# Performance work log

Measured on AMD Instinct MI355X. Metric: run time of the kernel, lower is better.

## Reference

```python
import jax, jax.numpy as jnp
import numpy as np

B, T, D, H, NL = 8, 1024, 512, 8, 3
WS = (3, 5, 7)


def _mha(q_in, k_in, v_in, wq, bq, wk, bk, wv, bv, wo, bo):
    """Faithful copy of the torch MultiHeadAttention, including the
    transpose-free .view(B*H, -1, dh) head split (row-major reshape)."""
    bs = q_in.shape[0]
    dh = D // H
    q = (q_in @ wq + bq).reshape(bs * H, -1, dh)
    k = (k_in @ wk + bk).reshape(bs * H, -1, dh)
    v = (v_in @ wv + bv).reshape(bs * H, -1, dh)
    scores = jnp.einsum('bqd,bkd->bqk', q, k) / (dh ** 0.5)
    weights = jax.nn.softmax(scores, axis=-1)
    att = jnp.einsum('bqk,bkd->bqd', weights, v).reshape(bs, -1, D)
    return att @ wo + bo


def _forward(x, loc_wq, loc_bq, loc_wk, loc_bk, loc_wv, loc_bv, loc_wo, loc_bo,
             g_wq, g_bq, g_wk, g_bk, g_wv, g_bv, g_wo, g_bo, out_w, out_b):
    feats = []
    for lv in range(NL):
        w = WS[lv]
        pad = (w - 1) // 2
        xp = jnp.pad(x, ((0, 0), (pad, pad), (0, 0)))  # [B, T+2p, D]
        idx = jnp.arange(T)[:, None] + jnp.arange(w)[None, :]  # [T, w]
        win = xp[:, idx, :].reshape(B * T, w, D)  # sliding windows, same as unfold+permute
        lo = _mha(win, win, win,
                  loc_wq[lv], loc_bq[lv], loc_wk[lv], loc_bk[lv],
                  loc_wv[lv], loc_bv[lv], loc_wo[lv], loc_bo[lv])
        feats.append(lo.reshape(B, T, w, D).mean(axis=2))
    feats.append(_mha(x, x, x, g_wq, g_bq, g_wk, g_bk, g_wv, g_bv, g_wo, g_bo))
    combined = jnp.concatenate(feats, axis=-1)  # [B, T, D*(NL+1)]
    return combined @ out_w + out_b  # dropout is identity in eval mode


def setup_inputs() -> dict:
    key = jax.random.key(0)
    ks = jax.random.split(key, 20)
    s = 0.02
    d = {}
    d['x'] = jax.random.normal(ks[0], (B, T, D), jnp.float32)
    d['loc_wq'] = jax.random.normal(ks[1], (NL, D, D), jnp.float32) * s
    d['loc_bq'] = jax.random.normal(ks[2], (NL, D), jnp.float32) * s
    d['loc_wk'] = jax.random.normal(ks[3], (NL, D, D), jnp.float32) * s
    d['loc_bk'] = jax.random.normal(ks[4], (NL, D), jnp.float32) * s
    d['loc_wv'] = jax.random.normal(ks[5], (NL, D, D), jnp.float32) * s
    d['loc_bv'] = jax.random.normal(ks[6], (NL, D), jnp.float32) * s
    d['loc_wo'] = jax.random.normal(ks[7], (NL, D, D), jnp.float32) * s
    d['loc_bo'] = jax.random.normal(ks[8], (NL, D), jnp.float32) * s
    d['g_wq'] = jax.random.normal(ks[9], (D, D), jnp.float32) * s
    d['g_bq'] = jax.random.normal(ks[10], (D,), jnp.float32) * s
    d['g_wk'] = jax.random.normal(ks[11], (D, D), jnp.float32) * s
    d['g_bk'] = jax.random.normal(ks[12], (D,), jnp.float32) * s
    d['g_wv'] = jax.random.normal(ks[13], (D, D), jnp.float32) * s
    d['g_bv'] = jax.random.normal(ks[14], (D,), jnp.float32) * s
    d['g_wo'] = jax.random.normal(ks[15], (D, D), jnp.float32) * s
    d['g_bo'] = jax.random.normal(ks[16], (D,), jnp.float32) * s
    d['out_w'] = jax.random.normal(ks[17], (D * (NL + 1), D), jnp.float32) * s
    d['out_b'] = jax.random.normal(ks[18], (D,), jnp.float32) * s
    return d


def reference(x, loc_wq, loc_bq, loc_wk, loc_bk, loc_wv, loc_bv, loc_wo, loc_bo,
              g_wq, g_bq, g_wk, g_bk, g_wv, g_bv, g_wo, g_bo, out_w, out_b):
    return _forward(x, loc_wq, loc_bq, loc_wk, loc_bk, loc_wv, loc_bv, loc_wo, loc_bo,
                    g_wq, g_bq, g_wk, g_bk, g_wv, g_bv, g_wo, g_bo, out_w, out_b)
```

## Files before the change

kernel.cpp:

```cpp
#include <hip/hip_runtime.h>
#include <hip/hip_bf16.h>
#include <cstddef>

#define T_SEQ 1024
#define D_MODEL 512

typedef __attribute__((ext_vector_type(8))) __bf16 bf16x8;
typedef __attribute__((ext_vector_type(4))) float f32x4;
typedef __attribute__((ext_vector_type(16))) float f32x16;
typedef __attribute__((ext_vector_type(8))) unsigned short u16x8;
typedef __attribute__((ext_vector_type(4))) unsigned int u32x4;

typedef const unsigned int __attribute__((address_space(1)))* gas1_t;
typedef unsigned int __attribute__((address_space(3)))* las3_t;

__device__ __forceinline__ void gload_lds16(const void* g, void* l) {
  __builtin_amdgcn_global_load_lds((gas1_t)g, (las3_t)l, 16, 0, 0);
}

__device__ __forceinline__ float bf2f(unsigned short u) {
  return __uint_as_float(((unsigned)u) << 16);
}
__device__ __forceinline__ unsigned short f2bf(float f) {
  __hip_bfloat16 h = __float2bfloat16(f);
  return *(unsigned short*)&h;
}

#define CVTPK(dst, a, b) \
  asm("v_cvt_pk_bf16_f32 %0, %1, %2" : "=v"(dst) : "v"(a), "v"(b))

__device__ __forceinline__ void swap32(unsigned& a, unsigned& b, int lane) {
  const unsigned ax = __shfl_xor(a, 32);
  const unsigned bx = __shfl_xor(b, 32);
  const bool lo = lane < 32;
  const unsigned na = lo ? a : bx;
  const unsigned nb = lo ? ax : b;
  a = na; b = nb;
}

__global__ __launch_bounds__(256)
void prep_weights_kernel(const float* __restrict__ loc_wq, const float* __restrict__ loc_wk,
                         const float* __restrict__ loc_wv, const float* __restrict__ g_wq,
                         const float* __restrict__ g_wk, const float* __restrict__ g_wv,
                         const float* __restrict__ out_w, const float* __restrict__ loc_wo,
                         const float* __restrict__ g_wo, const float* __restrict__ x,
                         const float* __restrict__ loc_bq, const float* __restrict__ loc_bk,
                         const float* __restrict__ loc_bv,
                         __hip_bfloat16* __restrict__ WT, __hip_bfloat16* __restrict__ xb,
                         __hip_bfloat16* __restrict__ bqkvb) {
  __shared__ float tile[32][33];
  const size_t MS = (size_t)512 * 512;
  const int z = blockIdx.y;
  const int t = threadIdx.x;

  if (z == 20) {
    const int base = blockIdx.x * 16384 + t * 8;
#pragma unroll
    for (int it = 0; it < 8; ++it) {
      const int i = base + it * 2048;
      const float4 a = *(const float4*)(x + i);
      const float4 b = *(const float4*)(x + i + 4);
      u16x8 o;
      o[0] = f2bf(a.x); o[1] = f2bf(a.y); o[2] = f2bf(a.z); o[3] = f2bf(a.w);
      o[4] = f2bf(b.x); o[5] = f2bf(b.y); o[6] = f2bf(b.z); o[7] = f2bf(b.w);
      *(u16x8*)(xb + i) = o;
    }
    return;
  }
  if (z == 21) {
    const int i = blockIdx.x * 256 + t;
    if (blockIdx.x < 18) {
      const int which = i >> 9, lv = which / 3, role = which % 3, e = i & 511;
      const float* src = role == 0 ? loc_bq : role == 1 ? loc_bk : loc_bv;
      bqkvb[i] = __float2bfloat16(src[lv * 512 + e]);
    }
    return;
  }

  const float* src;
  bool tr = true;
  if (z < 3)       src = loc_wq + (size_t)z * MS;
  else if (z < 6)  src = loc_wk + (size_t)(z - 3) * MS;
  else if (z < 9)  src = loc_wv + (size_t)(z - 6) * MS;
  else if (z == 9)  src = g_wq;
  else if (z == 10) src = g_wk;
  else if (z == 11) src = g_wv;
  else if (z < 16) src = out_w + (size_t)(z - 12) * MS;
  else if (z < 19) { src = loc_wo + (size_t)(z - 16) * MS; tr = false; }
  else             { src = g_wo; tr = false; }
  __hip_bfloat16* dst = WT + (size_t)z * MS;

  const int tk = (blockIdx.x & 15) * 32;
  const int tn = (blockIdx.x >> 4) * 32;
  const int r = t >> 3, c4 = (t & 7) * 4;
  const float4 v = *(const float4*)(src + (size_t)(tk + r) * 512 + tn + c4);
  if (tr) {
    tile[r][c4 + 0] = v.x; tile[r][c4 + 1] = v.y;
    tile[r][c4 + 2] = v.z; tile[r][c4 + 3] = v.w;
    __syncthreads();
    ushort4 o;
    o.x = f2bf(tile[c4 + 0][r]); o.y = f2bf(tile[c4 + 1][r]);
    o.z = f2bf(tile[c4 + 2][r]); o.w = f2bf(tile[c4 + 3][r]);
    *(ushort4*)(dst + (size_t)(tn + r) * 512 + tk + c4) = o;
  } else {
    ushort4 o;
    o.x = f2bf(v.x); o.y = f2bf(v.y); o.z = f2bf(v.z); o.w = f2bf(v.w);
    *(ushort4*)(dst + (size_t)(tk + r) * 512 + tn + c4) = o;
  }
}

__global__ __launch_bounds__(256)
void bias_fuse_kernel(const float* __restrict__ loc_bo, const float* __restrict__ g_bo,
                      const float* __restrict__ out_w, const float* __restrict__ out_b,
                      float* __restrict__ bfused) {
  const int z = blockIdx.y;
  const int n = blockIdx.x * 256 + threadIdx.x;
  const float* bo = (z < 3) ? loc_bo + z * 512 : g_bo;
  const float* W = out_w + (size_t)z * 512 * 512;
  float acc = (z == 0) ? out_b[n] : 0.f;
  for (int m = 0; m < 512; ++m)
    acc = fmaf(bo[m], W[(size_t)m * 512 + n], acc);
  bfused[z * 512 + n] = acc;
}

__device__ __forceinline__ void gemm_core_b128(
    const __hip_bfloat16* __restrict__ A, const __hip_bfloat16* __restrict__ BT,
    __hip_bfloat16* As, __hip_bfloat16* Bs, int row0, int col0, f32x4 acc[4][4]) {
  const int tid = threadIdx.x;
  const int wv = tid >> 6, lane = tid & 63;
  const int g = lane >> 4, r16 = lane & 15;
  const int wm = wv >> 1, wn = wv & 1;
  const char* Ab = (const char*)A;
  const char* Bb = (const char*)BT;
  for (int k0 = 0; k0 < 512; k0 += 32) {
    {
      const int row = tid >> 2, off = (tid & 3) << 4;
      gload_lds16(Ab + (size_t)(row0 + row) * 1024 + k0 * 2 + off,
                  (char*)As + (wv << 10));
      const int i2 = tid + 256;
      const int row2 = i2 >> 2, off2 = (i2 & 3) << 4;
      gload_lds16(Ab + (size_t)(row0 + row2) * 1024 + k0 * 2 + off2,
                  (char*)As + 4096 + (wv << 10));
    }
    {
      const int row = tid >> 2, off = (tid & 3) << 4;
      gload_lds16(Bb + (size_t)(col0 + row) * 1024 + k0 * 2 + off,
                  (char*)Bs + (wv << 10));
      const int i2 = tid + 256;
      const int row2 = i2 >> 2, off2 = (i2 & 3) << 4;
      gload_lds16(Bb + (size_t)(col0 + row2) * 1024 + k0 * 2 + off2,
                  (char*)Bs + 4096 + (wv << 10));
    }
    __syncthreads();
    bf16x8 a[4], b[4];
#pragma unroll
    for (int m = 0; m < 4; ++m)
      a[m] = *(const bf16x8*)(As + (wm * 64 + m * 16 + r16) * 32 + g * 8);
#pragma unroll
    for (int n = 0; n < 4; ++n)
      b[n] = *(const bf16x8*)(Bs + (wn * 64 + n * 16 + r16) * 32 + g * 8);
#pragma unroll
    for (int m = 0; m < 4; ++m)
#pragma unroll
      for (int n = 0; n < 4; ++n)
        acc[m][n] = __builtin_amdgcn_mfma_f32_16x16x32_bf16(a[m], b[n], acc[m][n], 0, 0, 0);
    __syncthreads();
  }
}

__device__ __forceinline__ void gemm_core_b64(
    const __hip_bfloat16* __restrict__ A, const __hip_bfloat16* __restrict__ BT,
    __hip_bfloat16* As, __hip_bfloat16* Bs, int row0, int col0, f32x4 acc[2][4]) {
  const int tid = threadIdx.x;
  const int wv = tid >> 6, lane = tid & 63;
  const int g = lane >> 4, r16 = lane & 15;
  const int wm = wv >> 1, wn = wv & 1;
  const char* Ab = (const char*)A;
  const char* Bb = (const char*)BT;
  for (int k0 = 0; k0 < 512; k0 += 32) {
    {
      const int row = tid >> 2, off = (tid & 3) << 4;
      gload_lds16(Ab + (size_t)(row0 + row) * 1024 + k0 * 2 + off,
                  (char*)As + (wv << 10));
    }
    {
      const int row = tid >> 2, off = (tid & 3) << 4;
      gload_lds16(Bb + (size_t)(col0 + row) * 1024 + k0 * 2 + off,
                  (char*)Bs + (wv << 10));
      const int i2 = tid + 256;
      const int row2 = i2 >> 2, off2 = (i2 & 3) << 4;
      gload_lds16(Bb + (size_t)(col0 + row2) * 1024 + k0 * 2 + off2,
                  (char*)Bs + 4096 + (wv << 10));
    }
    __syncthreads();
    bf16x8 a[2], b[4];
#pragma unroll
    for (int m = 0; m < 2; ++m)
      a[m] = *(const bf16x8*)(As + (wm * 32 + m * 16 + r16) * 32 + g * 8);
#pragma unroll
    for (int n = 0; n < 4; ++n)
      b[n] = *(const bf16x8*)(Bs + (wn * 64 + n * 16 + r16) * 32 + g * 8);
#pragma unroll
    for (int m = 0; m < 2; ++m)
#pragma unroll
      for (int n = 0; n < 4; ++n)
        acc[m][n] = __builtin_amdgcn_mfma_f32_16x16x32_bf16(a[m], b[n], acc[m][n], 0, 0, 0);
    __syncthreads();
  }
}

__global__ __launch_bounds__(256)
void gemm_qkv_kernel(const __hip_bfloat16* __restrict__ A,
                     const __hip_bfloat16* __restrict__ WT_base, size_t wt_stride,
                     const float* __restrict__ b0, const float* __restrict__ b1,
                     const float* __restrict__ b2,
                     __hip_bfloat16* __restrict__ out_base) {
  __shared__ __attribute__((aligned(16))) __hip_bfloat16 As[4096];
  __shared__ __attribute__((aligned(16))) __hip_bfloat16 Bs[4096];
  const int z = blockIdx.z;
  const __hip_bfloat16* WT = WT_base + (size_t)z * wt_stride;
  const float* bias = (z == 0) ? b0 : (z == 1) ? b1 : b2;
  __hip_bfloat16* C = out_base + (size_t)z * (size_t)(8192 * 512);
  const int row0 = blockIdx.y * 128, col0 = blockIdx.x * 128;
  f32x4 acc[4][4];
#pragma unroll
  for (int m = 0; m < 4; ++m)
#pragma unroll
    for (int n = 0; n < 4; ++n) acc[m][n] = (f32x4)(0.0f);
  gemm_core_b128(A, WT, As, Bs, row0, col0, acc);
  const int lane = threadIdx.x & 63, wv = threadIdx.x >> 6;
  const int g = lane >> 4, r16 = lane & 15, wm = wv >> 1, wn = wv & 1;
#pragma unroll
  for (int n = 0; n < 4; ++n) {
    const int col = col0 + wn * 64 + n * 16 + r16;
    const float bn = bias[col];
#pragma unroll
    for (int m = 0; m < 4; ++m) {
      const int rowb = row0 + wm * 64 + m * 16 + g * 4;
#pragma unroll
      for (int r = 0; r < 4; ++r)
        C[(size_t)(rowb + r) * 512 + col] = __float2bfloat16(acc[m][n][r] + bn);
    }
  }
}

__global__ __launch_bounds__(256)
void gemm_fusew_kernel(const __hip_bfloat16* __restrict__ A_base,
                       const __hip_bfloat16* __restrict__ BT_base,
                       __hip_bfloat16* __restrict__ C_base) {
  __shared__ __attribute__((aligned(16))) __hip_bfloat16 As[4096];
  __shared__ __attribute__((aligned(16))) __hip_bfloat16 Bs[4096];
  const size_t MS = (size_t)512 * 512;
  const int z = blockIdx.z;
  const __hip_bfloat16* A = A_base + z * MS;
  const __hip_bfloat16* BT = BT_base + z * MS;
  __hip_bfloat16* C = C_base + z * MS;
  const int row0 = blockIdx.y * 128, col0 = blockIdx.x * 128;
  f32x4 acc[4][4];
#pragma unroll
  for (int m = 0; m < 4; ++m)
#pragma unroll
    for (int n = 0; n < 4; ++n) acc[m][n] = (f32x4)(0.0f);
  gemm_core_b128(A, BT, As, Bs, row0, col0, acc);
  const int lane = threadIdx.x & 63, wv = threadIdx.x >> 6;
  const int g = lane >> 4, r16 = lane & 15, wm = wv >> 1, wn = wv & 1;
#pragma unroll
  for (int n = 0; n < 4; ++n) {
    const int col = col0 + wn * 64 + n * 16 + r16;
#pragma unroll
    for (int m = 0; m < 4; ++m) {
      const int rowb = row0 + wm * 64 + m * 16 + g * 4;
#pragma unroll
      for (int r = 0; r < 4; ++r)
        C[(size_t)(rowb + r) * 512 + col] = __float2bfloat16(acc[m][n][r]);
    }
  }
}

__global__ __launch_bounds__(256)
void gemm_out_fused_kernel(const __hip_bfloat16* __restrict__ A0,
                           const __hip_bfloat16* __restrict__ A1,
                           const __hip_bfloat16* __restrict__ A2,
                           const __hip_bfloat16* __restrict__ A3,
                           const __hip_bfloat16* __restrict__ WT_base,
                           const float* __restrict__ bfused,
                           float* __restrict__ out) {
  __shared__ __attribute__((aligned(16))) __hip_bfloat16 As[2048];
  __shared__ __attribute__((aligned(16))) __hip_bfloat16 Bs[4096];
  const size_t MS = (size_t)512 * 512;
  const int row0 = blockIdx.y * 64, col0 = blockIdx.x * 128;
  f32x4 acc[2][4];
#pragma unroll
  for (int m = 0; m < 2; ++m)
#pragma unroll
    for (int n = 0; n < 4; ++n) acc[m][n] = (f32x4)(0.0f);
  const __hip_bfloat16* Az[4] = {A0, A1, A2, A3};
  for (int z = 0; z < 4; ++z)
    gemm_core_b64(Az[z], WT_base + (size_t)z * MS, As, Bs, row0, col0, acc);
  const int lane = threadIdx.x & 63, wv = threadIdx.x >> 6;
  const int g = lane >> 4, r16 = lane & 15, wm = wv >> 1, wn = wv & 1;
#pragma unroll
  for (int n = 0; n < 4; ++n) {
    const int col = col0 + wn * 64 + n * 16 + r16;
    const float bn = bfused[col] + bfused[512 + col] + bfused[1024 + col] +
                     bfused[1536 + col];
#pragma unroll
    for (int m = 0; m < 2; ++m) {
      const int rowb = row0 + wm * 32 + m * 16 + g * 4;
#pragma unroll
      for (int r = 0; r < 4; ++r)
        out[(size_t)(rowb + r) * 512 + col] = acc[m][n][r] + bn;
    }
  }
}

template <int W>
__device__ __forceinline__ const __hip_bfloat16* slot_row(
    const __hip_bfloat16* __restrict__ X, const __hip_bfloat16* __restrict__ biasb,
    int b, int tloc, int pg, int sl, int* ch_out) {
  constexpr int PAD = (W - 1) / 2;
  const int hloc = sl >> 3, p = sl & 7;
  const int m = (pg * 4 + hloc) * W + p;
  const int j = m >> 3;
  *ch_out = m & 7;
  int sr = tloc + j - PAD;
  if (p < W) {
    if (sr >= 0 && sr < T_SEQ) return X + ((size_t)(b * T_SEQ + sr) << 9);
    return biasb;
  }
  sr = sr < 0 ? 0 : (sr > T_SEQ - 1 ? T_SEQ - 1 : sr);
  return X + ((size_t)(b * T_SEQ + sr) << 9);
}

template <int W>
__global__ __launch_bounds__(256)
void local_attn_mfma_kernel(const __hip_bfloat16* __restrict__ Xq,
                            const __hip_bfloat16* __restrict__ Xk,
                            const __hip_bfloat16* __restrict__ Xv,
                            const __hip_bfloat16* __restrict__ bqb,
                            const __hip_bfloat16* __restrict__ bkb,
                            const __hip_bfloat16* __restrict__ bvb,
                            __hip_bfloat16* __restrict__ abar) {
  __shared__ unsigned lds_u[4][2048];
  const int tid = threadIdx.x;
  const int wv = tid >> 6, lane = tid & 63;
  const int bt = blockIdx.x * 4 + wv;
  const int b = bt >> 10, tloc = bt & 1023;
  unsigned* L = &lds_u[wv][0];
  const int dl = lane & 31, hi = lane >> 5;

  {
    const int k2 = dl, dhalf = hi;
    int ch0, ch1;
    const __hip_bfloat16* r0 =
        slot_row<W>(Xv, bvb, b, tloc, (2 * k2) >> 5, (2 * k2) & 31, &ch0);
    const __hip_bfloat16* r1 =
        slot_row<W>(Xv, bvb, b, tloc, (2 * k2 + 1) >> 5, (2 * k2 + 1) & 31, &ch1);
    u16x8 A0[4], A1[4];
#pragma unroll
    for (int q = 0; q < 4; ++q) {
      A0[q] = *(const u16x8*)(r0 + ch0 * 64 + dhalf * 32 + q * 8);
      A1[q] = *(const u16x8*)(r1 + ch1 * 64 + dhalf * 32 + q * 8);
    }
#pragma unroll
    for (int q = 0; q < 4; ++q)
#pragma unroll
      for (int e = 0; e < 8; ++e) {
        const int d_ = dhalf * 32 + q * 8 + e;
        const unsigned dw = (unsigned)A0[q][e] | ((unsigned)A1[q][e] << 16);
        const int byte = (d_ * 128 + k2 * 4) ^ ((d_ & 7) << 4);
        L[byte >> 2] = dw;
      }
  }

  f32x16 accP[2][2];
#pragma unroll
  for (int pg = 0; pg < 2; ++pg)
#pragma unroll
    for (int dh = 0; dh < 2; ++dh) accP[pg][dh] = (f32x16)(0.0f);

  const int myb = dl >> 3;

#pragma unroll
  for (int pg = 0; pg < 2; ++pg) {
    int chK, chQ;
    const __hip_bfloat16* rK = slot_row<W>(Xk, bkb, b, tloc, pg, dl, &chK);
    const __hip_bfloat16* rQ = slot_row<W>(Xq, bqb, b, tloc, pg, dl, &chQ);
    f32x16 sa = (f32x16)(0.0f);
#pragma unroll
    for (int i = 0; i < 4; ++i) {
      const bf16x8 kf = *(const bf16x8*)(rK + chK * 64 + i * 16 + hi * 8);
      const bf16x8 qf = *(const bf16x8*)(rQ + chQ * 64 + i * 16 + hi * 8);
      sa = __builtin_amdgcn_mfma_f32_32x32x16_bf16(kf, qf, sa, 0, 0, 0);
    }

    float sel[4];
#pragma unroll
    for (int r4 = 0; r4 < 4; ++r4)
      sel[r4] = (myb == 0) ? sa[r4]
              : (myb == 1) ? sa[4 + r4]
              : (myb == 2) ? sa[8 + r4] : sa[12 + r4];

    float mx = -3e38f;
#pragma unroll
    for (int r4 = 0; r4 < 4; ++r4)
      if (r4 + 4 * hi < W) mx = fmaxf(mx, sel[r4]);
    mx = fmaxf(mx, __shfl_xor(mx, 32));
    float e[4], ls = 0.f;
#pragma unroll
    for (int r4 = 0; r4 < 4; ++r4) {
      e[r4] = (r4 + 4 * hi < W) ? __expf(0.125f * (sel[r4] - mx)) : 0.f;
      ls += e[r4];
    }
    ls += __shfl_xor(ls, 32);
    const float inv = 1.f / ls;

    unsigned dw0, dw1;
    CVTPK(dw0, e[0] * inv, e[1] * inv);
    CVTPK(dw1, e[2] * inv, e[3] * inv);
    const unsigned q0 = __shfl_xor(dw0, 32);
    const unsigned q1 = __shfl_xor(dw1, 32);

#pragma unroll
    for (int kh = 0; kh < 2; ++kh) {
      const bool on = (2 * kh + hi) == myb;
      u32x4 bw;
      if (hi == 0) { bw[0] = dw0; bw[1] = dw1; bw[2] = q0; bw[3] = q1; }
      else         { bw[0] = q0;  bw[1] = q1;  bw[2] = dw0; bw[3] = dw1; }
      if (!on) { bw[0] = 0u; bw[1] = 0u; bw[2] = 0u; bw[3] = 0u; }
      const bf16x8 pf = __builtin_bit_cast(bf16x8, bw);
#pragma unroll
      for (int dh = 0; dh < 2; ++dh) {
        const int d_ = dh * 32 + dl;
        const int off = (d_ * 128 + pg * 64 + kh * 32 + hi * 16) ^ ((d_ & 7) << 4);
        const bf16x8 va =
            __builtin_bit_cast(bf16x8, *(const u32x4*)((const char*)L + off));
        accP[pg][dh] = __builtin_amdgcn_mfma_f32_32x32x16_bf16(va, pf, accP[pg][dh], 0, 0, 0);
      }
    }
  }

#pragma unroll
  for (int pg = 0; pg < 2; ++pg) {
    if ((dl & 7) < W) {
      const int m_o = (pg * 4 + (dl >> 3)) * W + (dl & 7);
#pragma unroll
      for (int dh = 0; dh < 2; ++dh) {
#pragma unroll
        for (int rq = 0; rq < 4; ++rq) {
          unsigned wa, wb;
          CVTPK(wa, accP[pg][dh][4 * rq + 0], accP[pg][dh][4 * rq + 1]);
          CVTPK(wb, accP[pg][dh][4 * rq + 2], accP[pg][dh][4 * rq + 3]);
          const int dwi = m_o * 34 + dh * 16 + rq * 4 + hi * 2;
          uint2 w; w.x = wa; w.y = wb;
          *(uint2*)(L + dwi) = w;
        }
      }
    }
  }
  asm volatile("s_waitcnt lgkmcnt(0)" ::: "memory");

  const int cho = lane >> 3, fb = lane & 7;
  float o[8] = {0.f, 0.f, 0.f, 0.f, 0.f, 0.f, 0.f, 0.f};
#pragma unroll
  for (int jj = 0; jj < W; ++jj) {
    const int mo = 8 * jj + cho;
    const uint2 w0 = *(const uint2*)(L + mo * 34 + fb * 4);
    const uint2 w1 = *(const uint2*)(L + mo * 34 + fb * 4 + 2);
    o[0] += bf2f((unsigned short)(w0.x & 0xffff));
    o[1] += bf2f((unsigned short)(w0.x >> 16));
    o[2] += bf2f((unsigned short)(w0.y & 0xffff));
    o[3] += bf2f((unsigned short)(w0.y >> 16));
    o[4] += bf2f((unsigned short)(w1.x & 0xffff));
    o[5] += bf2f((unsigned short)(w1.x >> 16));
    o[6] += bf2f((unsigned short)(w1.y & 0xffff));
    o[7] += bf2f((unsigned short)(w1.y >> 16));
  }
  const float invw = 1.f / (float)W;
  u16x8 ov;
#pragma unroll
  for (int e2 = 0; e2 < 8; ++e2) ov[e2] = f2bf(o[e2] * invw);
  *(u16x8*)(abar + ((size_t)bt << 9) + cho * 64 + fb * 8) = ov;
}

__global__ __launch_bounds__(256)
void global_attn_mfma_kernel(const __hip_bfloat16* __restrict__ Xq,
                             const __hip_bfloat16* __restrict__ Xk,
                             const __hip_bfloat16* __restrict__ Xv,
                             __hip_bfloat16* __restrict__ att) {
  __shared__ unsigned vt[2][2048];
  const int tid = threadIdx.x;
  const int lane = tid & 63;
  const int wv = tid >> 6;
  const int qblk = blockIdx.x;
  const int bh = blockIdx.y;
  const size_t base = (size_t)bh << 16;
  const int c = lane & 31;
  const int g = lane >> 5;
  const int q0 = qblk * 128 + wv * 32;

  const __hip_bfloat16* Qp = Xq + base;
  const __hip_bfloat16* Kp = Xk + base;
  const __hip_bfloat16* Vp = Xv + base;

  bf16x8 qf[4];
#pragma unroll
  for (int s = 0; s < 4; ++s)
    qf[s] = *(const bf16x8*)(Qp + (size_t)(q0 + c) * 64 + s * 16 + g * 8);

  const int k2 = tid & 31, dblk = tid >> 5;

  bf16x8 kf[2][4];
  u16x8 v0, v1, v0n, v1n;

  v0 = *(const u16x8*)(Vp + (size_t)(2 * k2) * 64 + dblk * 8);
  v1 = *(const u16x8*)(Vp + (size_t)(2 * k2 + 1) * 64 + dblk * 8);
#pragma unroll
  for (int kb = 0; kb < 2; ++kb)
#pragma unroll
    for (int s = 0; s < 4; ++s)
      kf[kb][s] = *(const bf16x8*)(Kp + (size_t)(kb * 32 + c) * 64 + s * 16 + g * 8);

  f32x16 Oa = (f32x16)(0.0f), Ob = (f32x16)(0.0f);
  float m_run = -3e38f, l_run = 0.f;

  for (int kt = 0; kt < 16; ++kt) {
    unsigned* vb = &vt[kt & 1][0];
#pragma unroll
    for (int jj = 0; jj < 8; ++jj) {
      const int d = dblk * 8 + jj;
      const unsigned dw = (unsigned)v0[jj] | ((unsigned)v1[jj] << 16);
      const int byte = (d * 128 + k2 * 4) ^ ((d & 7) << 4);
      vb[byte >> 2] = dw;
    }
    if (kt < 15) {
      const __hip_bfloat16* vsrc = Vp + (size_t)((kt + 1) * 64 + 2 * k2) * 64 + dblk * 8;
      v0n = *(const u16x8*)vsrc;
      v1n = *(const u16x8*)(vsrc + 64);
    }
    __syncthreads();

    f32x16 sa = (f32x16)(0.0f), sb = (f32x16)(0.0f);
#pragma unroll
    for (int s = 0; s < 4; ++s)
      sa = __builtin_amdgcn_mfma_f32_32x32x16_bf16(kf[0][s], qf[s], sa, 0, 0, 0);
#pragma unroll
    for (int s = 0; s < 4; ++s)
      sb = __builtin_amdgcn_mfma_f32_32x32x16_bf16(kf[1][s], qf[s], sb, 0, 0, 0);

    if (kt < 15) {
#pragma unroll
      for (int kb = 0; kb < 2; ++kb)
#pragma unroll
        for (int s = 0; s < 4; ++s)
          kf[kb][s] = *(const bf16x8*)(Kp + (size_t)((kt + 1) * 64 + kb * 32 + c) * 64 +
                                       s * 16 + g * 8);
    }

    float mx = sa[0];
#pragma unroll
    for (int r = 1; r < 16; ++r) mx = fmaxf(mx, sa[r]);
#pragma unroll
    for (int r = 0; r < 16; ++r) mx = fmaxf(mx, sb[r]);
    mx = fmaxf(mx, __shfl_xor(mx, 32));
    const float m_new = fmaxf(m_run, mx * 0.125f);
    const float alpha = __expf(m_run - m_new);

    float p0[16], p1[16];
    float lsum = 0.f;
#pragma unroll
    for (int r = 0; r < 16; ++r) { p0[r] = __expf(fmaf(sa[r], 0.125f, -m_new)); lsum += p0[r]; }
#pragma unroll
    for (int r = 0; r < 16; ++r) { p1[r] = __expf(fmaf(sb[r], 0.125f, -m_new)); lsum += p1[r]; }
    lsum += __shfl_xor(lsum, 32);
    l_run = fmaf(l_run, alpha, lsum);
    m_run = m_new;
#pragma unroll
    for (int r = 0; r < 16; ++r) { Oa[r] *= alpha; Ob[r] *= alpha; }

    unsigned bw[2][2][4];
#define REDIST(pb, kb_)                                                  \
    {                                                                    \
      unsigned t0_, t1_, t2_, t3_, t4_, t5_, t6_, t7_;                   \
      CVTPK(t0_, pb[0], pb[1]);   CVTPK(t1_, pb[2], pb[3]);              \
      CVTPK(t2_, pb[4], pb[5]);   CVTPK(t3_, pb[6], pb[7]);              \
      CVTPK(t4_, pb[8], pb[9]);   CVTPK(t5_, pb[10], pb[11]);            \
      CVTPK(t6_, pb[12], pb[13]); CVTPK(t7_, pb[14], pb[15]);            \
      swap32(t0_, t2_, lane); swap32(t1_, t3_, lane);                    \
      swap32(t4_, t6_, lane); swap32(t5_, t7_, lane);                    \
      bw[kb_][0][0] = t0_; bw[kb_][0][1] = t1_; bw[kb_][0][2] = t2_;     \
      bw[kb_][0][3] = t3_;                                               \
      bw[kb_][1][0] = t4_; bw[kb_][1][1] = t5_; bw[kb_][1][2] = t6_;     \
      bw[kb_][1][3] = t7_;                                               \
    }
    REDIST(p0, 0)
    REDIST(p1, 1)
#undef REDIST

    const unsigned* vbr = &vt[kt & 1][0];
#pragma unroll
    for (int kb = 0; kb < 2; ++kb)
#pragma unroll
      for (int st = 0; st < 2; ++st) {
        const u32x4 pw = { bw[kb][st][0], bw[kb][st][1], bw[kb][st][2], bw[kb][st][3] };
        const bf16x8 pf = __builtin_bit_cast(bf16x8, pw);
        {
          const int row = c;
          const int off = (row * 128 + (kb * 64 + st * 32 + g * 16)) ^ ((row & 7) << 4);
          const bf16x8 va = __builtin_bit_cast(bf16x8, *(const u32x4*)((const char*)vbr + off));
          Oa = __builtin_amdgcn_mfma_f32_32x32x16_bf16(va, pf, Oa, 0, 0, 0);
        }
        {
          const int row = 32 + c;
          const int off = (row * 128 + (kb * 64 + st * 32 + g * 16)) ^ ((row & 7) << 4);
          const bf16x8 va = __builtin_bit_cast(bf16x8, *(const u32x4*)((const char*)vbr + off));
          Ob = __builtin_amdgcn_mfma_f32_32x32x16_bf16(va, pf, Ob, 0, 0, 0);
        }
      }

    v0 = v0n; v1 = v1n;
  }

  const float inv = 1.f / l_run;
  __hip_bfloat16* drow = att + base + (size_t)(q0 + c) * 64;
#pragma unroll
  for (int qd = 0; qd < 4; ++qd) {
    unsigned lo, hi2;
    {
      const float a0 = Oa[4 * qd + 0] * inv, a1 = Oa[4 * qd + 1] * inv;
      const float a2 = Oa[4 * qd + 2] * inv, a3 = Oa[4 * qd + 3] * inv;
      CVTPK(lo, a0, a1); CVTPK(hi2, a2, a3);
      uint2 w; w.x = lo; w.y = hi2;
      *(uint2*)(drow + 8 * qd + 4 * g) = w;
    }
    {
      const float a0 = Ob[4 * qd + 0] * inv, a1 = Ob[4 * qd + 1] * inv;
      const float a2 = Ob[4 * qd + 2] * inv, a3 = Ob[4 * qd + 3] * inv;
      CVTPK(lo, a0, a1); CVTPK(hi2, a2, a3);
      uint2 w; w.x = lo; w.y = hi2;
      *(uint2*)(drow + 32 + 8 * qd + 4 * g) = w;
    }
  }
}

extern "C" void kernel_launch(void* const* d_in, const int* in_sizes, int n_in,
                              void* d_out, int out_size, void* d_ws, size_t ws_size,
                              hipStream_t stream) {
  const float* x      = (const float*)d_in[0];
  const float* loc_wq = (const float*)d_in[1];
  const float* loc_bq = (const float*)d_in[2];
  const float* loc_wk = (const float*)d_in[3];
  const float* loc_bk = (const float*)d_in[4];
  const float* loc_wv = (const float*)d_in[5];
  const float* loc_bv = (const float*)d_in[6];
  const float* loc_wo = (const float*)d_in[7];
  const float* loc_bo = (const float*)d_in[8];
  const float* g_wq  = (const float*)d_in[9];
  const float* g_bq  = (const float*)d_in[10];
  const float* g_wk  = (const float*)d_in[11];
  const float* g_bk  = (const float*)d_in[12];
  const float* g_wv  = (const float*)d_in[13];
  const float* g_bv  = (const float*)d_in[14];
  const float* g_wo  = (const float*)d_in[15];
  const float* g_bo  = (const float*)d_in[16];
  const float* out_w = (const float*)d_in[17];
  const float* out_b = (const float*)d_in[18];
  float* out = (float*)d_out;

  __hip_bfloat16* wsb = (__hip_bfloat16*)d_ws;
  const size_t SZ = (size_t)8192 * 512;
  const size_t MS = (size_t)512 * 512;
  __hip_bfloat16* xb    = wsb;
  __hip_bfloat16* WT    = wsb + SZ;
  __hip_bfloat16* Xq    = wsb + SZ + 24 * MS;
  __hip_bfloat16* Xk    = Xq + SZ;
  __hip_bfloat16* Xv    = Xq + 2 * SZ;
  __hip_bfloat16* abar0 = Xq + 3 * SZ;
  __hip_bfloat16* abar1 = Xq + 4 * SZ;
  __hip_bfloat16* abar2 = Xq + 5 * SZ;
  __hip_bfloat16* abar3 = Xq + 6 * SZ;
  float* bfused = (float*)(Xq + 7 * SZ);
  __hip_bfloat16* bqkvb = (__hip_bfloat16*)(bfused + 2048);
  __hip_bfloat16* abars[3] = {abar0, abar1, abar2};

  const dim3 thr(256);

  prep_weights_kernel<<<dim3(256, 22), thr, 0, stream>>>(
      loc_wq, loc_wk, loc_wv, g_wq, g_wk, g_wv, out_w, loc_wo, g_wo,
      x, loc_bq, loc_bk, loc_bv, WT, xb, bqkvb);
  gemm_fusew_kernel<<<dim3(4, 4, 4), thr, 0, stream>>>(WT + 12 * MS, WT + 16 * MS,
                                                       WT + 20 * MS);
  bias_fuse_kernel<<<dim3(2, 4), thr, 0, stream>>>(loc_bo, g_bo, out_w, out_b, bfused);

  const dim3 gqkv(4, 64, 3);

  for (int lv = 0; lv < 3; ++lv) {
    gemm_qkv_kernel<<<gqkv, thr, 0, stream>>>(
        xb, WT + lv * MS, 3 * MS,
        loc_bq + lv * 512, loc_bk + lv * 512, loc_bv + lv * 512, Xq);

    const __hip_bfloat16* bqb = bqkvb + (lv * 3 + 0) * 512;
    const __hip_bfloat16* bkb = bqkvb + (lv * 3 + 1) * 512;
    const __hip_bfloat16* bvb = bqkvb + (lv * 3 + 2) * 512;
    if (lv == 0)
      local_attn_mfma_kernel<3><<<2048, thr, 0, stream>>>(Xq, Xk, Xv, bqb, bkb, bvb, abars[lv]);
    else if (lv == 1)
      local_attn_mfma_kernel<5><<<2048, thr, 0, stream>>>(Xq, Xk, Xv, bqb, bkb, bvb, abars[lv]);
    else
      local_attn_mfma_kernel<7><<<2048, thr, 0, stream>>>(Xq, Xk, Xv, bqb, bkb, bvb, abars[lv]);
  }

  gemm_qkv_kernel<<<gqkv, thr, 0, stream>>>(xb, WT + 9 * MS, MS, g_bq, g_bk, g_bv, Xq);
  global_attn_mfma_kernel<<<dim3(8, 64), thr, 0, stream>>>(Xq, Xk, Xv, abar3);

  gemm_out_fused_kernel<<<dim3(4, 128), thr, 0, stream>>>(abar0, abar1, abar2, abar3,
                                                          WT + 20 * MS, bfused, out);
}
```

Baseline: 290.1 us.

## Batch all QKV projections into one launch, add lazy rescale and MFMA priority

Adds a single QKV GEMM launch that computes all twelve projections (three local levels plus global) at once when the workspace is large enough, replacing four smaller launches. It also restructures global attention to process two key tiles per sync, skips the online-softmax rescale when no lane's max grows, and raises wave priority around MFMA blocks in both attention kernels. The aim is fewer launches, better GPU fill, fewer barriers and fewer rescale multiplies, at the cost of much more workspace memory and a fallback path when the workspace is too small.

```diff
diff --git a/kernel.cpp b/kernel.cpp
--- a/kernel.cpp
+++ b/kernel.cpp
@@ -245,6 +245,47 @@
 }
 
 __global__ __launch_bounds__(256)
+void gemm_qkv_all_kernel(const __hip_bfloat16* __restrict__ A,
+                         const __hip_bfloat16* __restrict__ WT_base,
+                         const float* __restrict__ loc_bq, const float* __restrict__ loc_bk,
+                         const float* __restrict__ loc_bv, const float* __restrict__ g_bq,
+                         const float* __restrict__ g_bk, const float* __restrict__ g_bv,
+                         __hip_bfloat16* __restrict__ proj_base) {
+  __shared__ __attribute__((aligned(16))) __hip_bfloat16 As[4096];
+  __shared__ __attribute__((aligned(16))) __hip_bfloat16 Bs[4096];
+  const size_t MS = (size_t)512 * 512;
+  const int z = blockIdx.z;
+  const __hip_bfloat16* WT = WT_base + (size_t)z * MS;
+  const float* bias;
+  if (z < 3)       bias = loc_bq + z * 512;
+  else if (z < 6)  bias = loc_bk + (z - 3) * 512;
+  else if (z < 9)  bias = loc_bv + (z - 6) * 512;
+  else             bias = (z == 9) ? g_bq : (z == 10) ? g_bk : g_bv;
+  __hip_bfloat16* C = proj_base + (size_t)z * (size_t)(8192 * 512);
+  const int row0 = blockIdx.y * 128, col0 = blockIdx.x * 128;
+  f32x4 acc[4][4];
+#pragma unroll
+  for (int m = 0; m < 4; ++m)
+#pragma unroll
+    for (int n = 0; n < 4; ++n) acc[m][n] = (f32x4)(0.0f);
+  gemm_core_b128(A, WT, As, Bs, row0, col0, acc);
+  const int lane = threadIdx.x & 63, wv = threadIdx.x >> 6;
+  const int g = lane >> 4, r16 = lane & 15, wm = wv >> 1, wn = wv & 1;
+#pragma unroll
+  for (int n = 0; n < 4; ++n) {
+    const int col = col0 + wn * 64 + n * 16 + r16;
+    const float bn = bias[col];
+#pragma unroll
+    for (int m = 0; m < 4; ++m) {
+      const int rowb = row0 + wm * 64 + m * 16 + g * 4;
+#pragma unroll
+      for (int r = 0; r < 4; ++r)
+        C[(size_t)(rowb + r) * 512 + col] = __float2bfloat16(acc[m][n][r] + bn);
+    }
+  }
+}
+
+__global__ __launch_bounds__(256)
 void gemm_fusew_kernel(const __hip_bfloat16* __restrict__ A_base,
                        const __hip_bfloat16* __restrict__ BT_base,
                        __hip_bfloat16* __restrict__ C_base) {
@@ -387,12 +428,14 @@
     const __hip_bfloat16* rK = slot_row<W>(Xk, bkb, b, tloc, pg, dl, &chK);
     const __hip_bfloat16* rQ = slot_row<W>(Xq, bqb, b, tloc, pg, dl, &chQ);
     f32x16 sa = (f32x16)(0.0f);
+    __builtin_amdgcn_s_setprio(1);
 #pragma unroll
     for (int i = 0; i < 4; ++i) {
       const bf16x8 kf = *(const bf16x8*)(rK + chK * 64 + i * 16 + hi * 8);
       const bf16x8 qf = *(const bf16x8*)(rQ + chQ * 64 + i * 16 + hi * 8);
       sa = __builtin_amdgcn_mfma_f32_32x32x16_bf16(kf, qf, sa, 0, 0, 0);
     }
+    __builtin_amdgcn_s_setprio(0);
 
     float sel[4];
 #pragma unroll
@@ -421,6 +464,7 @@
     const unsigned q0 = __shfl_xor(dw0, 32);
     const unsigned q1 = __shfl_xor(dw1, 32);
 
+    __builtin_amdgcn_s_setprio(1);
 #pragma unroll
     for (int kh = 0; kh < 2; ++kh) {
       const bool on = (2 * kh + hi) == myb;
@@ -438,6 +482,7 @@
         accP[pg][dh] = __builtin_amdgcn_mfma_f32_32x32x16_bf16(va, pf, accP[pg][dh], 0, 0, 0);
       }
     }
+    __builtin_amdgcn_s_setprio(0);
   }
 
 #pragma unroll
@@ -483,102 +528,6 @@
   *(u16x8*)(abar + ((size_t)bt << 9) + cho * 64 + fb * 8) = ov;
 }
 
-__global__ __launch_bounds__(256)
-void global_attn_mfma_kernel(const __hip_bfloat16* __restrict__ Xq,
-                             const __hip_bfloat16* __restrict__ Xk,
-                             const __hip_bfloat16* __restrict__ Xv,
-                             __hip_bfloat16* __restrict__ att) {
-  __shared__ unsigned vt[2][2048];
-  const int tid = threadIdx.x;
-  const int lane = tid & 63;
-  const int wv = tid >> 6;
-  const int qblk = blockIdx.x;
-  const int bh = blockIdx.y;
-  const size_t base = (size_t)bh << 16;
-  const int c = lane & 31;
-  const int g = lane >> 5;
-  const int q0 = qblk * 128 + wv * 32;
-
-  const __hip_bfloat16* Qp = Xq + base;
-  const __hip_bfloat16* Kp = Xk + base;
-  const __hip_bfloat16* Vp = Xv + base;
-
-  bf16x8 qf[4];
-#pragma unroll
-  for (int s = 0; s < 4; ++s)
-    qf[s] = *(const bf16x8*)(Qp + (size_t)(q0 + c) * 64 + s * 16 + g * 8);
-
-  const int k2 = tid & 31, dblk = tid >> 5;
-
-  bf16x8 kf[2][4];
-  u16x8 v0, v1, v0n, v1n;
-
-  v0 = *(const u16x8*)(Vp + (size_t)(2 * k2) * 64 + dblk * 8);
-  v1 = *(const u16x8*)(Vp + (size_t)(2 * k2 + 1) * 64 + dblk * 8);
-#pragma unroll
-  for (int kb = 0; kb < 2; ++kb)
-#pragma unroll
-    for (int s = 0; s < 4; ++s)
-      kf[kb][s] = *(const bf16x8*)(Kp + (size_t)(kb * 32 + c) * 64 + s * 16 + g * 8);
-
-  f32x16 Oa = (f32x16)(0.0f), Ob = (f32x16)(0.0f);
-  float m_run = -3e38f, l_run = 0.f;
-
-  for (int kt = 0; kt < 16; ++kt) {
-    unsigned* vb = &vt[kt & 1][0];
-#pragma unroll
-    for (int jj = 0; jj < 8; ++jj) {
-      const int d = dblk * 8 + jj;
-      const unsigned dw = (unsigned)v0[jj] | ((unsigned)v1[jj] << 16);
-      const int byte = (d * 128 + k2 * 4) ^ ((d & 7) << 4);
-      vb[byte >> 2] = dw;
-    }
-    if (kt < 15) {
-      const __hip_bfloat16* vsrc = Vp + (size_t)((kt + 1) * 64 + 2 * k2) * 64 + dblk * 8;
-      v0n = *(const u16x8*)vsrc;
-      v1n = *(const u16x8*)(vsrc + 64);
-    }
-    __syncthreads();
-
-    f32x16 sa = (f32x16)(0.0f), sb = (f32x16)(0.0f);
-#pragma unroll
-    for (int s = 0; s < 4; ++s)
-      sa = __builtin_amdgcn_mfma_f32_32x32x16_bf16(kf[0][s], qf[s], sa, 0, 0, 0);
-#pragma unroll
-    for (int s = 0; s < 4; ++s)
-      sb = __builtin_amdgcn_mfma_f32_32x32x16_bf16(kf[1][s], qf[s], sb, 0, 0, 0);
-
-    if (kt < 15) {
-#pragma unroll
-      for (int kb = 0; kb < 2; ++kb)
-#pragma unroll
-        for (int s = 0; s < 4; ++s)
-          kf[kb][s] = *(const bf16x8*)(Kp + (size_t)((kt + 1) * 64 + kb * 32 + c) * 64 +
-                                       s * 16 + g * 8);
-    }
-
-    float mx = sa[0];
-#pragma unroll
-    for (int r = 1; r < 16; ++r) mx = fmaxf(mx, sa[r]);
-#pragma unroll
-    for (int r = 0; r < 16; ++r) mx = fmaxf(mx, sb[r]);
-    mx = fmaxf(mx, __shfl_xor(mx, 32));
-    const float m_new = fmaxf(m_run, mx * 0.125f);
-    const float alpha = __expf(m_run - m_new);
-
-    float p0[16], p1[16];
-    float lsum = 0.f;
-#pragma unroll
-    for (int r = 0; r < 16; ++r) { p0[r] = __expf(fmaf(sa[r], 0.125f, -m_new)); lsum += p0[r]; }
-#pragma unroll
-    for (int r = 0; r < 16; ++r) { p1[r] = __expf(fmaf(sb[r], 0.125f, -m_new)); lsum += p1[r]; }
-    lsum += __shfl_xor(lsum, 32);
-    l_run = fmaf(l_run, alpha, lsum);
-    m_run = m_new;
-#pragma unroll
-    for (int r = 0; r < 16; ++r) { Oa[r] *= alpha; Ob[r] *= alpha; }
-
-    unsigned bw[2][2][4];
 #define REDIST(pb, kb_)                                                  \
     {                                                                    \
       unsigned t0_, t1_, t2_, t3_, t4_, t5_, t6_, t7_;                   \
@@ -593,32 +542,144 @@
       bw[kb_][1][0] = t4_; bw[kb_][1][1] = t5_; bw[kb_][1][2] = t6_;     \
       bw[kb_][1][3] = t7_;                                               \
     }
-    REDIST(p0, 0)
-    REDIST(p1, 1)
-#undef REDIST
-
-    const unsigned* vbr = &vt[kt & 1][0];
-#pragma unroll
-    for (int kb = 0; kb < 2; ++kb)
-#pragma unroll
-      for (int st = 0; st < 2; ++st) {
-        const u32x4 pw = { bw[kb][st][0], bw[kb][st][1], bw[kb][st][2], bw[kb][st][3] };
-        const bf16x8 pf = __builtin_bit_cast(bf16x8, pw);
-        {
-          const int row = c;
-          const int off = (row * 128 + (kb * 64 + st * 32 + g * 16)) ^ ((row & 7) << 4);
-          const bf16x8 va = __builtin_bit_cast(bf16x8, *(const u32x4*)((const char*)vbr + off));
-          Oa = __builtin_amdgcn_mfma_f32_32x32x16_bf16(va, pf, Oa, 0, 0, 0);
-        }
-        {
-          const int row = 32 + c;
-          const int off = (row * 128 + (kb * 64 + st * 32 + g * 16)) ^ ((row & 7) << 4);
-          const bf16x8 va = __builtin_bit_cast(bf16x8, *(const u32x4*)((const char*)vbr + off));
-          Ob = __builtin_amdgcn_mfma_f32_32x32x16_bf16(va, pf, Ob, 0, 0, 0);
-        }
-      }
-
-    v0 = v0n; v1 = v1n;
+
+#define SUBSTEP(KF, SUB)                                                        \
+  {                                                                             \
+    f32x16 sa = (f32x16)(0.0f), sb = (f32x16)(0.0f);                            \
+    __builtin_amdgcn_s_setprio(1);                                              \
+    _Pragma("unroll")                                                           \
+    for (int s = 0; s < 4; ++s)                                                 \
+      sa = __builtin_amdgcn_mfma_f32_32x32x16_bf16(KF[0][s], qf[s], sa, 0, 0, 0);\
+    _Pragma("unroll")                                                           \
+    for (int s = 0; s < 4; ++s)                                                 \
+      sb = __builtin_amdgcn_mfma_f32_32x32x16_bf16(KF[1][s], qf[s], sb, 0, 0, 0);\
+    __builtin_amdgcn_s_setprio(0);                                              \
+    const int ktn = 2 * it + (SUB) + 2;                                         \
+    if (ktn < 16) {                                                             \
+      _Pragma("unroll")                                                         \
+      for (int kb = 0; kb < 2; ++kb)                                            \
+        _Pragma("unroll")                                                       \
+        for (int s = 0; s < 4; ++s)                                             \
+          KF[kb][s] = *(const bf16x8*)(Kp + (size_t)(ktn * 64 + kb * 32 + c) * 64 + \
+                                       s * 16 + g * 8);                         \
+    }                                                                           \
+    float mx = sa[0];                                                           \
+    _Pragma("unroll")                                                           \
+    for (int r = 1; r < 16; ++r) mx = fmaxf(mx, sa[r]);                         \
+    _Pragma("unroll")                                                           \
+    for (int r = 0; r < 16; ++r) mx = fmaxf(mx, sb[r]);                         \
+    mx = fmaxf(mx, __shfl_xor(mx, 32));                                         \
+    const float mt = mx * 0.125f;                                               \
+    if (__any(mt > m_run)) {                                                    \
+      const float m_new = fmaxf(m_run, mt);                                     \
+      const float alpha = __expf(m_run - m_new);                                \
+      m_run = m_new;                                                            \
+      l_run *= alpha;                                                           \
+      _Pragma("unroll")                                                         \
+      for (int r = 0; r < 16; ++r) { Oa[r] *= alpha; Ob[r] *= alpha; }          \
+    }                                                                           \
+    float p0[16], p1[16];                                                       \
+    float lsum = 0.f;                                                           \
+    _Pragma("unroll")                                                           \
+    for (int r = 0; r < 16; ++r) { p0[r] = __expf(fmaf(sa[r], 0.125f, -m_run)); lsum += p0[r]; } \
+    _Pragma("unroll")                                                           \
+    for (int r = 0; r < 16; ++r) { p1[r] = __expf(fmaf(sb[r], 0.125f, -m_run)); lsum += p1[r]; } \
+    lsum += __shfl_xor(lsum, 32);                                               \
+    l_run += lsum;                                                              \
+    unsigned bw[2][2][4];                                                       \
+    REDIST(p0, 0)                                                               \
+    REDIST(p1, 1)                                                               \
+    const unsigned* vbr = &vt[it & 1][(SUB)][0];                                \
+    __builtin_amdgcn_s_setprio(1);                                              \
+    _Pragma("unroll")                                                           \
+    for (int kb = 0; kb < 2; ++kb)                                              \
+      _Pragma("unroll")                                                         \
+      for (int st = 0; st < 2; ++st) {                                          \
+        const u32x4 pw = { bw[kb][st][0], bw[kb][st][1], bw[kb][st][2], bw[kb][st][3] }; \
+        const bf16x8 pf = __builtin_bit_cast(bf16x8, pw);                       \
+        {                                                                       \
+          const int row = c;                                                    \
+          const int off = (row * 128 + (kb * 64 + st * 32 + g * 16)) ^ ((row & 7) << 4); \
+          const bf16x8 va = __builtin_bit_cast(bf16x8, *(const u32x4*)((const char*)vbr + off)); \
+          Oa = __builtin_amdgcn_mfma_f32_32x32x16_bf16(va, pf, Oa, 0, 0, 0);    \
+        }                                                                       \
+        {                                                                       \
+          const int row = 32 + c;                                               \
+          const int off = (row * 128 + (kb * 64 + st * 32 + g * 16)) ^ ((row & 7) << 4); \
+          const bf16x8 va = __builtin_bit_cast(bf16x8, *(const u32x4*)((const char*)vbr + off)); \
+          Ob = __builtin_amdgcn_mfma_f32_32x32x16_bf16(va, pf, Ob, 0, 0, 0);    \
+        }                                                                       \
+      }                                                                         \
+    __builtin_amdgcn_s_setprio(0);                                              \
+  }
+
+__global__ __launch_bounds__(256)
+void global_attn_mfma_kernel(const __hip_bfloat16* __restrict__ Xq,
+                             const __hip_bfloat16* __restrict__ Xk,
+                             const __hip_bfloat16* __restrict__ Xv,
+                             __hip_bfloat16* __restrict__ att) {
+  __shared__ unsigned vt[2][2][2048];
+  const int tid = threadIdx.x;
+  const int lane = tid & 63;
+  const int wv = tid >> 6;
+  const int qblk = blockIdx.x;
+  const int bh = blockIdx.y;
+  const size_t base = (size_t)bh << 16;
+  const int c = lane & 31;
+  const int g = lane >> 5;
+  const int q0 = qblk * 128 + wv * 32;
+
+  const __hip_bfloat16* Qp = Xq + base;
+  const __hip_bfloat16* Kp = Xk + base;
+  const __hip_bfloat16* Vp = Xv + base;
+
+  bf16x8 qf[4];
+#pragma unroll
+  for (int s = 0; s < 4; ++s)
+    qf[s] = *(const bf16x8*)(Qp + (size_t)(q0 + c) * 64 + s * 16 + g * 8);
+
+  const int k2 = tid & 31, dblk = tid >> 5;
+
+  bf16x8 kfA[2][4], kfB[2][4];
+  u16x8 vA0, vA1, vB0, vB1;
+
+  vA0 = *(const u16x8*)(Vp + (size_t)(2 * k2) * 64 + dblk * 8);
+  vA1 = *(const u16x8*)(Vp + (size_t)(2 * k2 + 1) * 64 + dblk * 8);
+  vB0 = *(const u16x8*)(Vp + (size_t)(64 + 2 * k2) * 64 + dblk * 8);
+  vB1 = *(const u16x8*)(Vp + (size_t)(64 + 2 * k2 + 1) * 64 + dblk * 8);
+#pragma unroll
+  for (int kb = 0; kb < 2; ++kb)
+#pragma unroll
+    for (int s = 0; s < 4; ++s) {
+      kfA[kb][s] = *(const bf16x8*)(Kp + (size_t)(kb * 32 + c) * 64 + s * 16 + g * 8);
+      kfB[kb][s] = *(const bf16x8*)(Kp + (size_t)(64 + kb * 32 + c) * 64 + s * 16 + g * 8);
+    }
+
+  f32x16 Oa = (f32x16)(0.0f), Ob = (f32x16)(0.0f);
+  float m_run = -3e38f, l_run = 0.f;
+
+  for (int it = 0; it < 8; ++it) {
+    unsigned* vb0 = &vt[it & 1][0][0];
+    unsigned* vb1 = &vt[it & 1][1][0];
+#pragma unroll
+    for (int jj = 0; jj < 8; ++jj) {
+      const int d = dblk * 8 + jj;
+      const int byte = (d * 128 + k2 * 4) ^ ((d & 7) << 4);
+      vb0[byte >> 2] = (unsigned)vA0[jj] | ((unsigned)vA1[jj] << 16);
+      vb1[byte >> 2] = (unsigned)vB0[jj] | ((unsigned)vB1[jj] << 16);
+    }
+    if (it < 7) {
+      const __hip_bfloat16* sA = Vp + (size_t)((2 * it + 2) * 64 + 2 * k2) * 64 + dblk * 8;
+      vA0 = *(const u16x8*)sA;
+      vA1 = *(const u16x8*)(sA + 64);
+      const __hip_bfloat16* sB = Vp + (size_t)((2 * it + 3) * 64 + 2 * k2) * 64 + dblk * 8;
+      vB0 = *(const u16x8*)sB;
+      vB1 = *(const u16x8*)(sB + 64);
+    }
+    __syncthreads();
+
+    SUBSTEP(kfA, 0)
+    SUBSTEP(kfB, 1)
   }
 
   const float inv = 1.f / l_run;
@@ -670,18 +731,15 @@
   __hip_bfloat16* wsb = (__hip_bfloat16*)d_ws;
   const size_t SZ = (size_t)8192 * 512;
   const size_t MS = (size_t)512 * 512;
+
   __hip_bfloat16* xb    = wsb;
   __hip_bfloat16* WT    = wsb + SZ;
-  __hip_bfloat16* Xq    = wsb + SZ + 24 * MS;
-  __hip_bfloat16* Xk    = Xq + SZ;
-  __hip_bfloat16* Xv    = Xq + 2 * SZ;
-  __hip_bfloat16* abar0 = Xq + 3 * SZ;
-  __hip_bfloat16* abar1 = Xq + 4 * SZ;
-  __hip_bfloat16* abar2 = Xq + 5 * SZ;
-  __hip_bfloat16* abar3 = Xq + 6 * SZ;
-  float* bfused = (float*)(Xq + 7 * SZ);
-  __hip_bfloat16* bqkvb = (__hip_bfloat16*)(bfused + 2048);
-  __hip_bfloat16* abars[3] = {abar0, abar1, abar2};
+  float* bfused = (float*)(wsb + SZ + 24 * MS);
+  __hip_bfloat16* bqkvb = wsb + SZ + 24 * MS + 4096;
+  __hip_bfloat16* proj  = wsb + SZ + 24 * MS + 16384;
+
+  const size_t need_big = 2 * (17 * SZ + 24 * MS + 16384);
+  const bool big = ws_size >= need_big;
 
   const dim3 thr(256);
 
@@ -692,26 +750,53 @@
                                                        WT + 20 * MS);
   bias_fuse_kernel<<<dim3(2, 4), thr, 0, stream>>>(loc_bo, g_bo, out_w, out_b, bfused);
 
-  const dim3 gqkv(4, 64, 3);
-
-  for (int lv = 0; lv < 3; ++lv) {
-    gemm_qkv_kernel<<<gqkv, thr, 0, stream>>>(
-        xb, WT + lv * MS, 3 * MS,
-        loc_bq + lv * 512, loc_bk + lv * 512, loc_bv + lv * 512, Xq);
-
-    const __hip_bfloat16* bqb = bqkvb + (lv * 3 + 0) * 512;
-    const __hip_bfloat16* bkb = bqkvb + (lv * 3 + 1) * 512;
-    const __hip_bfloat16* bvb = bqkvb + (lv * 3 + 2) * 512;
-    if (lv == 0)
-      local_attn_mfma_kernel<3><<<2048, thr, 0, stream>>>(Xq, Xk, Xv, bqb, bkb, bvb, abars[lv]);
-    else if (lv == 1)
-      local_attn_mfma_kernel<5><<<2048, thr, 0, stream>>>(Xq, Xk, Xv, bqb, bkb, bvb, abars[lv]);
-    else
-      local_attn_mfma_kernel<7><<<2048, thr, 0, stream>>>(Xq, Xk, Xv, bqb, bkb, bvb, abars[lv]);
-  }
-
-  gemm_qkv_kernel<<<gqkv, thr, 0, stream>>>(xb, WT + 9 * MS, MS, g_bq, g_bk, g_bv, Xq);
-  global_attn_mfma_kernel<<<dim3(8, 64), thr, 0, stream>>>(Xq, Xk, Xv, abar3);
+  __hip_bfloat16 *abar0, *abar1, *abar2, *abar3;
+
+  if (big) {
+    abar0 = proj + 12 * SZ;
+    abar1 = proj + 13 * SZ;
+    abar2 = proj + 14 * SZ;
+    abar3 = proj + 15 * SZ;
+    gemm_qkv_all_kernel<<<dim3(4, 64, 12), thr, 0, stream>>>(
+        xb, WT, loc_bq, loc_bk, loc_bv, g_bq, g_bk, g_bv, proj);
+    local_attn_mfma_kernel<3><<<2048, thr, 0, stream>>>(
+        proj + 0 * SZ, proj + 3 * SZ, proj + 6 * SZ,
+        bqkvb + 0 * 512, bqkvb + 1 * 512, bqkvb + 2 * 512, abar0);
+    local_attn_mfma_kernel<5><<<2048, thr, 0, stream>>>(
+        proj + 1 * SZ, proj + 4 * SZ, proj + 7 * SZ,
+        bqkvb + 3 * 512, bqkvb + 4 * 512, bqkvb + 5 * 512, abar1);
+    local_attn_mfma_kernel<7><<<2048, thr, 0, stream>>>(
+        proj + 2 * SZ, proj + 5 * SZ, proj + 8 * SZ,
+        bqkvb + 6 * 512, bqkvb + 7 * 512, bqkvb + 8 * 512, abar2);
+    global_attn_mfma_kernel<<<dim3(8, 64), thr, 0, stream>>>(
+        proj + 9 * SZ, proj + 10 * SZ, proj + 11 * SZ, abar3);
+  } else {
+    __hip_bfloat16* Xq = proj;
+    __hip_bfloat16* Xk = proj + SZ;
+    __hip_bfloat16* Xv = proj + 2 * SZ;
+    abar0 = proj + 3 * SZ;
+    abar1 = proj + 4 * SZ;
+    abar2 = proj + 5 * SZ;
+    abar3 = proj + 6 * SZ;
+    __hip_bfloat16* abars[3] = {abar0, abar1, abar2};
+    const dim3 gqkv(4, 64, 3);
+    for (int lv = 0; lv < 3; ++lv) {
+      gemm_qkv_kernel<<<gqkv, thr, 0, stream>>>(
+          xb, WT + lv * MS, 3 * MS,
+          loc_bq + lv * 512, loc_bk + lv * 512, loc_bv + lv * 512, Xq);
+      const __hip_bfloat16* bqb = bqkvb + (lv * 3 + 0) * 512;
+      const __hip_bfloat16* bkb = bqkvb + (lv * 3 + 1) * 512;
+      const __hip_bfloat16* bvb = bqkvb + (lv * 3 + 2) * 512;
+      if (lv == 0)
+        local_attn_mfma_kernel<3><<<2048, thr, 0, stream>>>(Xq, Xk, Xv, bqb, bkb, bvb, abars[lv]);
+      else if (lv == 1)
+        local_attn_mfma_kernel<5><<<2048, thr, 0, stream>>>(Xq, Xk, Xv, bqb, bkb, bvb, abars[lv]);
+      else
+        local_attn_mfma_kernel<7><<<2048, thr, 0, stream>>>(Xq, Xk, Xv, bqb, bkb, bvb, abars[lv]);
+    }
+    gemm_qkv_kernel<<<gqkv, thr, 0, stream>>>(xb, WT + 9 * MS, MS, g_bq, g_bk, g_bv, Xq);
+    global_attn_mfma_kernel<<<dim3(8, 64), thr, 0, stream>>>(Xq, Xk, Xv, abar3);
+  }
 
   gemm_out_fused_kernel<<<dim3(4, 128), thr, 0, stream>>>(abar0, abar1, abar2, abar3,
                                                           WT + 20 * MS, bfused, out);
```

Result: no change. 289.7 us (-0.1%).
